# Optimization experiments

Measured on AMD Instinct MI355X. Metric: run time of the kernel, lower is better.

The kernel has to match this reference:

```python
import jax, jax.numpy as jnp
import numpy as np

NINP, NC, NH = 34, 128, 512
B, S, T = 64, 2048, 400
EPS = 1e-10


def _lstm_cell(x, h, c, Wih, Whh, bih, bhh):
    # torch.nn.LSTMCell gate order: i, f, g, o
    g = x @ Wih.T + bih + h @ Whh.T + bhh
    i, f, gg, o = jnp.split(g, 4, axis=1)
    c2 = jax.nn.sigmoid(f) * c + jax.nn.sigmoid(i) * jnp.tanh(gg)
    h2 = jax.nn.sigmoid(o) * jnp.tanh(c2)
    return h2, c2


def _attend(keys, values, mask, query):
    # energy: [B, S]; mask: [B, S] float 0/1
    energy = jnp.einsum('bc,bsc->bs', query, keys) * mask
    energy = energy - (1.0 - mask) * 1e6
    e = jnp.exp(energy - energy.max(axis=1, keepdims=True)) * mask
    att = e / e.sum(axis=1, keepdims=True)
    ctx = jnp.einsum('bs,bsc->bc', att, values)
    return att, ctx


def setup_inputs() -> dict:
    key = jax.random.key(0)
    ks = jax.random.split(key, 32)
    def rn(k, shape, scale=0.05):
        return (jax.random.normal(k, shape) * scale).astype(jnp.float32)
    inp = {
        'keys': rn(ks[0], (B, S, NC), 1.0),
        'values': rn(ks[1], (B, S, NC), 1.0),
        'lens': jax.random.randint(ks[2], (B,), S // 2, S + 1),
        'inputs': jax.random.randint(ks[3], (B, T), 0, NINP),
        'emb': rn(ks[4], (NINP, NC)),
        'wq': rn(ks[5], (NC, NH)), 'bq': jnp.zeros((NC,), jnp.float32),
        'wc': rn(ks[6], (NC, NH + NC)), 'bc': jnp.zeros((NC,), jnp.float32),
        'b_out': jnp.zeros((NINP,), jnp.float32),
    }
    in_sizes = [2 * NC, NH, NH]
    for l in range(3):
        inp['w%d_ih' % l] = rn(ks[7 + 4 * l], (4 * NH, in_sizes[l]))
        inp['w%d_hh' % l] = rn(ks[8 + 4 * l], (4 * NH, NH))
        inp['b%d_ih' % l] = jnp.zeros((4 * NH,), jnp.float32)
        inp['b%d_hh' % l] = jnp.zeros((4 * NH,), jnp.float32)
        inp['h0_%d' % l] = jnp.zeros((NH,), jnp.float32)  # ALSTMCell h0 param (zero init)
        inp['c0_%d' % l] = jnp.zeros((NH,), jnp.float32)
    return inp


def reference(keys, values, lens, inputs, emb, wq, bq, wc, bc, b_out,
              w0_ih, w0_hh, b0_ih, b0_hh, h0_0, c0_0,
              w1_ih, w1_hh, b1_ih, b1_hh, h0_1, c0_1,
              w2_ih, w2_hh, b2_ih, b2_hh, h0_2, c0_2):
    mask = (jnp.arange(S)[None, :] < lens[:, None]).astype(keys.dtype)  # [B,S]
    h1 = jnp.broadcast_to(h0_0[None], (B, NH)); c1 = jnp.broadcast_to(c0_0[None], (B, NH))
    h2 = jnp.broadcast_to(h0_1[None], (B, NH)); c2 = jnp.broadcast_to(c0_1[None], (B, NH))
    h3 = jnp.broadcast_to(h0_2[None], (B, NH)); c3 = jnp.broadcast_to(c0_2[None], (B, NH))
    # initial attention from last layer's h0 (matches torch forward)
    query0 = h3 @ wq.T + bq
    _, ctx = _attend(keys, values, mask, query0)
    # precompute gumbel noise for all T steps: -log(eps - log(U + eps))
    U = jax.random.uniform(jax.random.key(1), (T, B, NINP), dtype=jnp.float32)
    gnoise = -jnp.log(EPS - jnp.log(U + EPS))

    def step(carry, xs):
        h1, c1, h2, c2, h3, c3, ctx = carry
        tok, gn = xs
        x = jnp.concatenate([emb[tok], ctx], axis=1)  # [B, 2*NC]
        h1, c1 = _lstm_cell(x, h1, c1, w0_ih, w0_hh, b0_ih, b0_hh)
        h2, c2 = _lstm_cell(h1, h2, c2, w1_ih, w1_hh, b1_ih, b1_hh)
        h3, c3 = _lstm_cell(h2, h3, c3, w2_ih, w2_hh, b2_ih, b2_hh)
        q = h3 @ wq.T + bq
        att, ctx = _attend(keys, values, mask, q)
        z = jax.nn.leaky_relu(jnp.concatenate([h3, ctx], axis=1) @ wc.T + bc, 0.01)
        logit = z @ emb.T + b_out  # tied output weight = embedding
        gen = jnp.argmax(logit + gn, axis=1)
        return (h1, c1, h2, c2, h3, c3, ctx), (logit, att, gen)

    _, (logits, attentions, generated) = jax.lax.scan(
        step, (h1, c1, h2, c2, h3, c3, ctx), (inputs.T, gnoise))
    return logits, attentions, generated
```

## Files before the change

### kernel.cpp

```cpp
#include <hip/hip_runtime.h>

#define NINP 34
#define NCC  128
#define NHH  512
#define BBB  64
#define SSS  2048
#define TTT  400
#define GEPS 1e-10f

#define GDIM 512
#define NTHR 256
#define NCHK 8
#define SCHK 256

#define JAX_PARTITIONABLE 1

#define OFF_H   0
#define OFF_C   196608
#define OFF_CTX 294912
#define OFF_ML  303104
#define OFF_P   303616

#define SY_ROOT 0
#define SY_GEN  16
#define SY_LEAFC(l) (256 + 8 * (l))
#define SY_LEAFG(l) (512 + 8 * (l))
#define SY_BF(b)    (1024 + 8 * (b))
#define SY_MF(b)    (1536 + 8 * (b))

struct Params {
  const float* keys; const float* values;
  const int* lens;  const int* toks;
  const float* emb; const float* wq; const float* bq;
  const float* wc;  const float* bc; const float* bout;
  const float* wih[3]; const float* whh[3];
  const float* bih[3]; const float* bhh[3];
  const float* h0[3];  const float* c0[3];
  float* out_logits; float* out_att; float* out_gen;
  float* wsf; unsigned* sync;
};

__device__ __forceinline__ float4 ld4(const float* p) { return *(const float4*)p; }
__device__ __forceinline__ float sigf(float x) { return 1.0f / (1.0f + expf(-x)); }

__device__ __forceinline__ unsigned aload(const unsigned* p) {
  return __hip_atomic_load(p, __ATOMIC_RELAXED, __HIP_MEMORY_SCOPE_AGENT);
}
__device__ __forceinline__ unsigned aadd(unsigned* p, unsigned v) {
  return __hip_atomic_fetch_add(p, v, __ATOMIC_RELAXED, __HIP_MEMORY_SCOPE_AGENT);
}
__device__ __forceinline__ void astore(unsigned* p, unsigned v) {
  __hip_atomic_store(p, v, __ATOMIC_RELAXED, __HIP_MEMORY_SCOPE_AGENT);
}
__device__ __forceinline__ float ldc(const float* p) {
  unsigned u = __hip_atomic_load((const unsigned*)p, __ATOMIC_RELAXED, __HIP_MEMORY_SCOPE_AGENT);
  return __uint_as_float(u);
}
__device__ __forceinline__ void stc(float* p, float v) {
  __hip_atomic_store((unsigned*)p, __float_as_uint(v), __ATOMIC_RELAXED, __HIP_MEMORY_SCOPE_AGENT);
}
__device__ __forceinline__ float4 ld4c(const float* p) {
  unsigned long long a = __hip_atomic_load((const unsigned long long*)p,
                                           __ATOMIC_RELAXED, __HIP_MEMORY_SCOPE_AGENT);
  unsigned long long b = __hip_atomic_load(((const unsigned long long*)p) + 1,
                                           __ATOMIC_RELAXED, __HIP_MEMORY_SCOPE_AGENT);
  float4 r;
  r.x = __uint_as_float((unsigned)a); r.y = __uint_as_float((unsigned)(a >> 32));
  r.z = __uint_as_float((unsigned)b); r.w = __uint_as_float((unsigned)(b >> 32));
  return r;
}
__device__ __forceinline__ void wait_vm0() {
  asm volatile("s_waitcnt vmcnt(0)" ::: "memory");
}
__device__ __forceinline__ void cbar() { asm volatile("" ::: "memory"); }

__device__ void gbar(unsigned* sync, unsigned& epoch, int bid) {
  wait_vm0();
  __syncthreads();
  if (threadIdx.x == 0) {
    epoch++;
    const int leaf = bid >> 4;
    const bool leader = (bid & 15) == 0;
    if (aadd(&sync[SY_LEAFC(leaf)], 1u) == 16u * epoch - 1u) {
      if (aadd(&sync[SY_ROOT], 1u) == 32u * epoch - 1u)
        astore(&sync[SY_GEN], epoch);
    }
    if (leader) {
      while (aload(&sync[SY_GEN]) < epoch) __builtin_amdgcn_s_sleep(1);
      astore(&sync[SY_LEAFG(leaf)], epoch);
    } else {
      while (aload(&sync[SY_LEAFG(leaf)]) < epoch) __builtin_amdgcn_s_sleep(1);
    }
  }
  __syncthreads();
  cbar();
}

__device__ __forceinline__ void waitflag(unsigned* p, unsigned target) {
  if (threadIdx.x == 0) {
    while (aload(p) < target) __builtin_amdgcn_s_sleep(2);
  }
  __syncthreads();
  cbar();
}
__device__ __forceinline__ void postflag(unsigned* p) {
  wait_vm0();
  __syncthreads();
  if (threadIdx.x == 0) aadd(p, 1u);
}

__device__ __forceinline__ void tfr(unsigned& x0, unsigned& x1, int r) {
  x0 += x1; x1 = (x1 << r) | (x1 >> (32 - r)); x1 ^= x0;
}
__device__ unsigned threefry_bits(unsigned idx) {
  const unsigned k0 = 0u, k1 = 1u;
  const unsigned k2 = 0x1BD11BDAu ^ k0 ^ k1;
#if JAX_PARTITIONABLE
  unsigned x0 = 0u, x1 = idx;
#else
  const unsigned half = (TTT * BBB * NINP) / 2;
  const bool lo = idx < half;
  unsigned x0 = lo ? idx : idx - half;
  unsigned x1 = lo ? idx + half : idx;
#endif
  x0 += k0; x1 += k1;
  tfr(x0,x1,13); tfr(x0,x1,15); tfr(x0,x1,26); tfr(x0,x1,6);
  x0 += k1; x1 += k2 + 1u;
  tfr(x0,x1,17); tfr(x0,x1,29); tfr(x0,x1,16); tfr(x0,x1,24);
  x0 += k2; x1 += k0 + 2u;
  tfr(x0,x1,13); tfr(x0,x1,15); tfr(x0,x1,26); tfr(x0,x1,6);
  x0 += k0; x1 += k1 + 3u;
  tfr(x0,x1,17); tfr(x0,x1,29); tfr(x0,x1,16); tfr(x0,x1,24);
  x0 += k1; x1 += k2 + 4u;
  tfr(x0,x1,13); tfr(x0,x1,15); tfr(x0,x1,26); tfr(x0,x1,6);
  x0 += k2; x1 += k0 + 5u;
#if JAX_PARTITIONABLE
  return x0 ^ x1;
#else
  return lo ? x0 : x1;
#endif
}
__device__ __forceinline__ float gumbel(unsigned idx) {
  unsigned bits = threefry_bits(idx);
  float u = __uint_as_float((bits >> 9) | 0x3f800000u) - 1.0f;
  u = fmaxf(u, 0.0f);
  return -logf(GEPS - logf(u + GEPS));
}

template<int L>
__device__ void lstm_layer(const Params& p, int t, const float* hin, float* hout,
                           float* sh, int up, int bh, int tid) {
  const float* hin_l = hin + L * BBB * NHH + (size_t)bh * 32 * NHH;
  float* houtl = hout + L * BBB * NHH;
  float* cl = p.wsf + OFF_C + L * BBB * NHH;
  const float* xlow = (L == 0) ? (const float*)0
                               : (hout + (L - 1) * BBB * NHH + (size_t)bh * 32 * NHH);

  const int insz = (L == 0) ? (2 * NCC) : NHH;
  const int nx = insz >> 7;
  const int nch = nx + 4;

  const int rhat = tid >> 5;
  const int bloc = tid & 31;
  const int g = rhat >> 1, jh = rhat & 1;
  const int j = 2 * up + jh;
  const int row = g * NHH + j;
  const float* wr  = p.wih[L] + (size_t)row * insz;
  const float* wr2 = p.whh[L] + (size_t)row * NHH;

  float* xb0 = sh;
  float* xb1 = sh + 4224;
  const int kk  = (tid & 31) << 2;
  const int rb0 = tid >> 5;

  float4 pf[4];
  auto issue = [&](int cc) {
#pragma unroll
    for (int it = 0; it < 4; ++it) {
      const int rb = rb0 + (it << 3);
      const int gb = bh * 32 + rb;
      const bool isx = cc < nx;
      const int off = (isx ? cc : cc - nx) << 7;
      if (L == 0) {
        if (isx) pf[it] = (cc == 0)
            ? ld4(p.emb + (size_t)p.toks[gb * TTT + t] * NCC + kk)
            : ld4c(p.wsf + OFF_CTX + gb * NCC + kk);
        else pf[it] = ld4c(hin_l + (size_t)rb * NHH + off + kk);
      } else {
        pf[it] = isx ? ld4c(xlow + (size_t)rb * NHH + off + kk)
                     : ld4c(hin_l + (size_t)rb * NHH + off + kk);
      }
    }
  };
  auto commit = [&](float* buf) {
#pragma unroll
    for (int it = 0; it < 4; ++it)
      *(float4*)&buf[(rb0 + (it << 3)) * 132 + kk] = pf[it];
  };

  float acc = p.bih[L][row] + p.bhh[L][row];
  float s0 = 0.f, s1 = 0.f, s2 = 0.f, s3 = 0.f;

  issue(0);
  commit(xb0);
  __syncthreads();
  for (int cc = 0; cc < nch; ++cc) {
    if (cc + 1 < nch) issue(cc + 1);
    const bool isx = cc < nx;
    const int off = (isx ? cc : cc - nx) << 7;
    const float* wp = (isx ? wr : wr2) + off;
    const float* xr = ((cc & 1) ? xb1 : xb0) + bloc * 132;
#pragma unroll 8
    for (int k = 0; k < 128; k += 4) {
      float4 w = ld4(wp + k);
      float4 x = ld4(xr + k);
      s0 = fmaf(w.x, x.x, s0); s1 = fmaf(w.y, x.y, s1);
      s2 = fmaf(w.z, x.z, s2); s3 = fmaf(w.w, x.w, s3);
    }
    if (cc + 1 < nch) commit((cc & 1) ? xb0 : xb1);
    __syncthreads();
  }
  acc += (s0 + s1) + (s2 + s3);

  float* gl = sh + 8448;
  gl[rhat * 32 + bloc] = acc;
  __syncthreads();
  if (tid < 64) {
    const int jh2 = tid >> 5, b2 = tid & 31;
    const int b = bh * 32 + b2;
    const int jj = 2 * up + jh2;
    const float iv = gl[(0 + jh2) * 32 + b2];
    const float fv = gl[(2 + jh2) * 32 + b2];
    const float gv = gl[(4 + jh2) * 32 + b2];
    const float ov = gl[(6 + jh2) * 32 + b2];
    const float cold = cl[(size_t)b * NHH + jj];
    const float cnew = sigf(fv) * cold + sigf(iv) * tanhf(gv);
    const float hnew = sigf(ov) * tanhf(cnew);
    cl[(size_t)b * NHH + jj] = cnew;
    stc(&houtl[(size_t)b * NHH + jj], hnew);
  }
}

__device__ void attend_phase(const Params& p, int a, int t, const float* h3,
                             float* sh, int bid, int tid, bool wout) {
  float* wsf = p.wsf;
  unsigned* sync = p.sync;
  const int b  = (bid & 7) * 8 + (bid >> 6);
  const int ch = (bid >> 3) & 7;
  const int sbase = ch * SCHK;

  float* us  = sh + 8704;
  float* qs  = sh + 9344;
  float* ps  = sh + 9472;
  float* red = sh + 9728;
  float* zs  = sh + 10784;
  float* lg  = sh + 10912;

  if (tid < 128) *(float4*)&us[tid * 4] = ld4c(h3 + (size_t)b * NHH + tid * 4);
  __syncthreads();
  if (tid < NCC) {
    const float* wr = p.wq + (size_t)tid * NHH;
    float s0 = 0.f, s1 = 0.f, s2 = 0.f, s3 = 0.f;
#pragma unroll 8
    for (int k = 0; k < NHH; k += 4) {
      float4 w = ld4(wr + k);
      s0 = fmaf(w.x, us[k],     s0); s1 = fmaf(w.y, us[k + 1], s1);
      s2 = fmaf(w.z, us[k + 2], s2); s3 = fmaf(w.w, us[k + 3], s3);
    }
    qs[tid] = p.bq[tid] + (s0 + s1) + (s2 + s3);
  }
  const int lenb = p.lens[b];
  __syncthreads();

  const int s = sbase + tid;
  const bool msk = s < lenb;
  float e = -1e6f;
  if (msk) {
    const float* kr = p.keys + ((size_t)b * SSS + s) * NCC;
    float e0 = 0.f, e1 = 0.f, e2 = 0.f, e3 = 0.f;
#pragma unroll 8
    for (int c = 0; c < NCC; c += 4) {
      float4 kv = ld4(kr + c);
      e0 = fmaf(qs[c],     kv.x, e0); e1 = fmaf(qs[c + 1], kv.y, e1);
      e2 = fmaf(qs[c + 2], kv.z, e2); e3 = fmaf(qs[c + 3], kv.w, e3);
    }
    e = (e0 + e1) + (e2 + e3);
  }

  float mx = e;
#pragma unroll
  for (int off = 32; off; off >>= 1) mx = fmaxf(mx, __shfl_xor(mx, off));
  if ((tid & 63) == 0) red[tid >> 6] = mx;
  __syncthreads();
  const float mc = fmaxf(fmaxf(red[0], red[1]), fmaxf(red[2], red[3]));
  const float pv = msk ? expf(e - mc) : 0.f;
  ps[tid] = pv;
  float ls = pv;
#pragma unroll
  for (int off = 32; off; off >>= 1) ls += __shfl_xor(ls, off);
  if ((tid & 63) == 0) red[4 + (tid >> 6)] = ls;
  __syncthreads();
  const float lc = (red[4] + red[5]) + (red[6] + red[7]);

  const int c4 = (tid & 31) << 2;
  const int sg = tid >> 5;
  float r0 = 0.f, r1 = 0.f, r2 = 0.f, r3 = 0.f;
  const int nval = min(max(lenb - sbase - sg * 32, 0), 32);
  const float* vb = p.values + ((size_t)b * SSS + sbase + sg * 32) * NCC + c4;
#pragma unroll 4
  for (int i2 = 0; i2 < nval; ++i2) {
    const float pw = ps[sg * 32 + i2];
    float4 vv = ld4(vb + (size_t)i2 * NCC);
    r0 = fmaf(pw, vv.x, r0); r1 = fmaf(pw, vv.y, r1);
    r2 = fmaf(pw, vv.z, r2); r3 = fmaf(pw, vv.w, r3);
  }
  __syncthreads();
  *(float4*)&red[sg * 132 + c4] = make_float4(r0, r1, r2, r3);
  __syncthreads();
  float* pout = wsf + OFF_P + ((size_t)b * NCHK + ch) * 132;
  if (tid < NCC) {
    float sum = 0.f;
#pragma unroll
    for (int sg2 = 0; sg2 < 8; ++sg2) sum += red[sg2 * 132 + tid];
    stc(&pout[2 + tid], sum);
  }
  if (tid == 0) { stc(&pout[0], mc); stc(&pout[1], lc); }
  postflag(&sync[SY_BF(b)]);

  float gm = 0.f, gL = 1.f;
  if (ch == 0) {
    waitflag(&sync[SY_BF(b)], (unsigned)(NCHK * (a + 1)));
    const float* pb = wsf + OFF_P + (size_t)b * NCHK * 132;
    if (tid < 8)       red[tid] = ldc(&pb[tid * 132]);
    else if (tid < 16) red[tid] = ldc(&pb[(tid - 8) * 132 + 1]);
    __syncthreads();
    float m = red[0];
#pragma unroll
    for (int i = 1; i < 8; ++i) m = fmaxf(m, red[i]);
    float L = 0.f;
#pragma unroll
    for (int i = 0; i < 8; ++i) L += red[8 + i] * expf(red[i] - m);
    gm = m; gL = L;
    if (tid < NCC) {
      float v = 0.f;
#pragma unroll
      for (int c2 = 0; c2 < NCHK; ++c2)
        v += ldc(&pb[c2 * 132 + 2 + tid]) * expf(red[c2] - m);
      v /= L;
      stc(&wsf[OFF_CTX + b * NCC + tid], v);
      us[NHH + tid] = v;
    }
    if (tid == 0) { stc(&wsf[OFF_ML + b * 8], m); stc(&wsf[OFF_ML + b * 8 + 1], L); }
    postflag(&sync[SY_MF(b)]);
  } else if (wout) {
    waitflag(&sync[SY_MF(b)], (unsigned)(a + 1));
    gm = ldc(&wsf[OFF_ML + b * 8]);
    gL = ldc(&wsf[OFF_ML + b * 8 + 1]);
  }

  if (wout) {
    float* ao = p.out_att + ((size_t)t * BBB + b) * SSS;
    ao[s] = (msk ? expf(e - gm) : 0.f) / gL;
    if (ch == 0) {
      if (tid < NCC) {
        const float* wr = p.wc + (size_t)tid * (NHH + NCC);
        float s0 = 0.f, s1 = 0.f, s2 = 0.f, s3 = 0.f;
#pragma unroll 8
        for (int k = 0; k < NHH + NCC; k += 4) {
          float4 w = ld4(wr + k);
          s0 = fmaf(w.x, us[k],     s0); s1 = fmaf(w.y, us[k + 1], s1);
          s2 = fmaf(w.z, us[k + 2], s2); s3 = fmaf(w.w, us[k + 3], s3);
        }
        float z = (s0 + s1) + (s2 + s3) + p.bc[tid];
        zs[tid] = (z >= 0.f) ? z : 0.01f * z;
      }
      __syncthreads();
      if (tid < NINP) {
        const float* er = p.emb + tid * NCC;
        float s0 = 0.f, s1 = 0.f, s2 = 0.f, s3 = 0.f;
#pragma unroll 8
        for (int k = 0; k < NCC; k += 4) {
          float4 w = ld4(er + k);
          s0 = fmaf(w.x, zs[k],     s0); s1 = fmaf(w.y, zs[k + 1], s1);
          s2 = fmaf(w.z, zs[k + 2], s2); s3 = fmaf(w.w, zs[k + 3], s3);
        }
        const float lgt = (s0 + s1) + (s2 + s3) + p.bout[tid];
        p.out_logits[((size_t)t * BBB + b) * NINP + tid] = lgt;
        lg[tid] = lgt + gumbel((unsigned)(t * (BBB * NINP) + b * NINP + tid));
      }
      __syncthreads();
      if (tid == 0) {
        float bv = lg[0]; int bix = 0;
        for (int i = 1; i < NINP; ++i) if (lg[i] > bv) { bv = lg[i]; bix = i; }
        p.out_gen[t * BBB + b] = (float)bix;
      }
      __syncthreads();
    }
  }
}

extern "C" __global__ void __launch_bounds__(NTHR, 2)
decoder_kernel(Params p) {
  __shared__ float sh[11008];
  const int bid = blockIdx.x;
  const int tid = threadIdx.x;
  const int up = (bid & 7) * 32 + (bid >> 4);
  const int bh = (bid >> 3) & 1;
  unsigned epoch = 0;
  unsigned* sync = p.sync;
  float* wsf = p.wsf;

  if (tid < 192) {
    const int l = tid >> 6, u = tid & 63;
    const int jh = u >> 5, b2 = u & 31;
    const int b = bh * 32 + b2;
    const int j = 2 * up + jh;
    stc(&wsf[OFF_H + ((size_t)l * BBB + b) * NHH + j], p.h0[l][j]);
    wsf[OFF_C + ((size_t)l * BBB + b) * NHH + j] = p.c0[l][j];
  }
  gbar(sync, epoch, bid);

  attend_phase(p, 0, -1, wsf + OFF_H + 2 * BBB * NHH, sh, bid, tid, false);
  gbar(sync, epoch, bid);

  for (int t = 0; t < TTT; ++t) {
    const float* hin = wsf + OFF_H + ((t & 1) ? 3 * BBB * NHH : 0);
    float* hout      = wsf + OFF_H + ((t & 1) ? 0 : 3 * BBB * NHH);

    lstm_layer<0>(p, t, hin, hout, sh, up, bh, tid);
    gbar(sync, epoch, bid);
    lstm_layer<1>(p, t, hin, hout, sh, up, bh, tid);
    gbar(sync, epoch, bid);
    lstm_layer<2>(p, t, hin, hout, sh, up, bh, tid);
    gbar(sync, epoch, bid);
    attend_phase(p, t + 1, t, hout + 2 * BBB * NHH, sh, bid, tid, true);
    gbar(sync, epoch, bid);
  }
}

extern "C" void kernel_launch(void* const* d_in, const int* in_sizes, int n_in,
                              void* d_out, int out_size, void* d_ws, size_t ws_size,
                              hipStream_t stream) {
  Params p;
  p.keys   = (const float*)d_in[0];
  p.values = (const float*)d_in[1];
  p.lens   = (const int*)d_in[2];
  p.toks   = (const int*)d_in[3];
  p.emb    = (const float*)d_in[4];
  p.wq     = (const float*)d_in[5];
  p.bq     = (const float*)d_in[6];
  p.wc     = (const float*)d_in[7];
  p.bc     = (const float*)d_in[8];
  p.bout   = (const float*)d_in[9];
  for (int l = 0; l < 3; ++l) {
    p.wih[l] = (const float*)d_in[10 + 6 * l];
    p.whh[l] = (const float*)d_in[11 + 6 * l];
    p.bih[l] = (const float*)d_in[12 + 6 * l];
    p.bhh[l] = (const float*)d_in[13 + 6 * l];
    p.h0[l]  = (const float*)d_in[14 + 6 * l];
    p.c0[l]  = (const float*)d_in[15 + 6 * l];
  }
  float* out = (float*)d_out;
  p.out_logits = out;
  p.out_att    = out + (size_t)TTT * BBB * NINP;
  p.out_gen    = out + (size_t)TTT * BBB * NINP + (size_t)TTT * BBB * SSS;
  p.sync = (unsigned*)d_ws;
  p.wsf  = (float*)((char*)d_ws + 8192);

  hipMemsetAsync(d_ws, 0, 8192, stream);
  decoder_kernel<<<dim3(GDIM), dim3(NTHR), 0, stream>>>(p);
}
```

Before: 47.55 ms.

## Retile LSTM layer work to 8 batches by 32 gate rows per block

```diff
diff --git a/kernel.cpp b/kernel.cpp
--- a/kernel.cpp
+++ b/kernel.cpp
@@ -149,53 +149,48 @@
 
 template<int L>
 __device__ void lstm_layer(const Params& p, int t, const float* hin, float* hout,
-                           float* sh, int up, int bh, int tid) {
-  const float* hin_l = hin + L * BBB * NHH + (size_t)bh * 32 * NHH;
+                           float* sh, int ug, int boct, int tid) {
+  const float* hin_l = hin + L * BBB * NHH + (size_t)boct * 8 * NHH;
   float* houtl = hout + L * BBB * NHH;
   float* cl = p.wsf + OFF_C + L * BBB * NHH;
   const float* xlow = (L == 0) ? (const float*)0
-                               : (hout + (L - 1) * BBB * NHH + (size_t)bh * 32 * NHH);
+                               : (hout + (L - 1) * BBB * NHH + (size_t)boct * 8 * NHH);
 
   const int insz = (L == 0) ? (2 * NCC) : NHH;
   const int nx = insz >> 7;
   const int nch = nx + 4;
 
-  const int rhat = tid >> 5;
-  const int bloc = tid & 31;
-  const int g = rhat >> 1, jh = rhat & 1;
-  const int j = 2 * up + jh;
+  const int rhat = tid >> 3;
+  const int bloc = tid & 7;
+  const int g = rhat >> 3, jl = rhat & 7;
+  const int j = ug * 8 + jl;
   const int row = g * NHH + j;
   const float* wr  = p.wih[L] + (size_t)row * insz;
   const float* wr2 = p.whh[L] + (size_t)row * NHH;
 
   float* xb0 = sh;
-  float* xb1 = sh + 4224;
+  float* xb1 = sh + 1056;
   const int kk  = (tid & 31) << 2;
   const int rb0 = tid >> 5;
 
-  float4 pf[4];
+  float4 pf;
   auto issue = [&](int cc) {
-#pragma unroll
-    for (int it = 0; it < 4; ++it) {
-      const int rb = rb0 + (it << 3);
-      const int gb = bh * 32 + rb;
-      const bool isx = cc < nx;
-      const int off = (isx ? cc : cc - nx) << 7;
-      if (L == 0) {
-        if (isx) pf[it] = (cc == 0)
-            ? ld4(p.emb + (size_t)p.toks[gb * TTT + t] * NCC + kk)
-            : ld4c(p.wsf + OFF_CTX + gb * NCC + kk);
-        else pf[it] = ld4c(hin_l + (size_t)rb * NHH + off + kk);
-      } else {
-        pf[it] = isx ? ld4c(xlow + (size_t)rb * NHH + off + kk)
-                     : ld4c(hin_l + (size_t)rb * NHH + off + kk);
-      }
+    const int rb = rb0;
+    const int gb = boct * 8 + rb;
+    const bool isx = cc < nx;
+    const int off = (isx ? cc : cc - nx) << 7;
+    if (L == 0) {
+      if (isx) pf = (cc == 0)
+          ? ld4(p.emb + (size_t)p.toks[gb * TTT + t] * NCC + kk)
+          : ld4c(p.wsf + OFF_CTX + gb * NCC + kk);
+      else pf = ld4c(hin_l + (size_t)rb * NHH + off + kk);
+    } else {
+      pf = isx ? ld4c(xlow + (size_t)rb * NHH + off + kk)
+               : ld4c(hin_l + (size_t)rb * NHH + off + kk);
     }
   };
   auto commit = [&](float* buf) {
-#pragma unroll
-    for (int it = 0; it < 4; ++it)
-      *(float4*)&buf[(rb0 + (it << 3)) * 132 + kk] = pf[it];
+    *(float4*)&buf[rb0 * 132 + kk] = pf;
   };
 
   float acc = p.bih[L][row] + p.bhh[L][row];
@@ -222,17 +217,17 @@
   }
   acc += (s0 + s1) + (s2 + s3);
 
-  float* gl = sh + 8448;
-  gl[rhat * 32 + bloc] = acc;
+  float* gl = sh + 2112;
+  gl[rhat * 8 + bloc] = acc;
   __syncthreads();
   if (tid < 64) {
-    const int jh2 = tid >> 5, b2 = tid & 31;
-    const int b = bh * 32 + b2;
-    const int jj = 2 * up + jh2;
-    const float iv = gl[(0 + jh2) * 32 + b2];
-    const float fv = gl[(2 + jh2) * 32 + b2];
-    const float gv = gl[(4 + jh2) * 32 + b2];
-    const float ov = gl[(6 + jh2) * 32 + b2];
+    const int jl2 = tid >> 3, bl = tid & 7;
+    const int b = boct * 8 + bl;
+    const int jj = ug * 8 + jl2;
+    const float iv = gl[(0  + jl2) * 8 + bl];
+    const float fv = gl[(8  + jl2) * 8 + bl];
+    const float gv = gl[(16 + jl2) * 8 + bl];
+    const float ov = gl[(24 + jl2) * 8 + bl];
     const float cold = cl[(size_t)b * NHH + jj];
     const float cnew = sigf(fv) * cold + sigf(iv) * tanhf(gv);
     const float hnew = sigf(ov) * tanhf(cnew);
@@ -404,17 +399,17 @@
   __shared__ float sh[11008];
   const int bid = blockIdx.x;
   const int tid = threadIdx.x;
-  const int up = (bid & 7) * 32 + (bid >> 4);
-  const int bh = (bid >> 3) & 1;
+  const int ug   = (bid & 7) * 8 + ((bid >> 3) & 7);
+  const int boct = bid >> 6;
   unsigned epoch = 0;
   unsigned* sync = p.sync;
   float* wsf = p.wsf;
 
   if (tid < 192) {
     const int l = tid >> 6, u = tid & 63;
-    const int jh = u >> 5, b2 = u & 31;
-    const int b = bh * 32 + b2;
-    const int j = 2 * up + jh;
+    const int jl = u >> 3, bl = u & 7;
+    const int b = boct * 8 + bl;
+    const int j = ug * 8 + jl;
     stc(&wsf[OFF_H + ((size_t)l * BBB + b) * NHH + j], p.h0[l][j]);
     wsf[OFF_C + ((size_t)l * BBB + b) * NHH + j] = p.c0[l][j];
   }
@@ -427,11 +422,11 @@
     const float* hin = wsf + OFF_H + ((t & 1) ? 3 * BBB * NHH : 0);
     float* hout      = wsf + OFF_H + ((t & 1) ? 0 : 3 * BBB * NHH);
 
-    lstm_layer<0>(p, t, hin, hout, sh, up, bh, tid);
+    lstm_layer<0>(p, t, hin, hout, sh, ug, boct, tid);
     gbar(sync, epoch, bid);
-    lstm_layer<1>(p, t, hin, hout, sh, up, bh, tid);
+    lstm_layer<1>(p, t, hin, hout, sh, ug, boct, tid);
     gbar(sync, epoch, bid);
-    lstm_layer<2>(p, t, hin, hout, sh, up, bh, tid);
+    lstm_layer<2>(p, t, hin, hout, sh, ug, boct, tid);
     gbar(sync, epoch, bid);
     attend_phase(p, t + 1, t, hout + 2 * BBB * NHH, sh, bid, tid, true);
     gbar(sync, epoch, bid);
```

Measured after the change: 43.23 ms. 9.1% less time.
